# Kernel optimization log

Hardware: AMD Instinct MI355X
Metric: run time of the kernel (lower is better)

Reference implementation:

```python
import jax, jax.numpy as jnp
import numpy as np

B, N, C_IN, C_OUT = 32, 4096, 16, 64
EMB, LINK, WIN = 16, 3, 12


def setup_inputs() -> dict:
    key = jax.random.key(0)
    ks = jax.random.split(key, 7)
    s = lambda k, shape, sc=1.0: jax.random.normal(k, shape, dtype=jnp.float32) * sc
    return {
        "x": s(ks[0], (B, N, C_IN)),
        "x_window": s(ks[1], (B, WIN, N, C_IN)),
        "node_embeddings": s(ks[2], (N, EMB)),
        "weights_pool": s(ks[3], (EMB, LINK, C_IN, C_OUT), 0.1),
        "weights_window": s(ks[4], (EMB, C_IN, C_OUT), 0.1),
        "bias_pool": s(ks[5], (EMB, C_OUT), 0.1),
        "T": s(ks[6], (WIN,), 0.1),
    }


def reference(x, x_window, node_embeddings, weights_pool, weights_window, bias_pool, T):
    # Adaptive adjacency: softmax over rows of relu(E E^T)   [N, N]
    n = node_embeddings.shape[0]
    supports = jax.nn.softmax(
        jax.nn.relu(node_embeddings @ node_embeddings.T), axis=1)
    # Chebyshev polynomial hops: T0=I, T1=A, Tk = 2*A*T(k-1) - T(k-2)
    support_set = [jnp.eye(n, dtype=supports.dtype), supports]
    for _ in range(2, weights_pool.shape[1]):
        support_set.append(2.0 * (supports @ support_set[-1]) - support_set[-2])
    supports_k = jnp.stack(support_set, axis=0)  # [K, N, N]

    # Per-node weight generation from node embeddings
    weights = jnp.einsum('nd,dkio->nkio', node_embeddings, weights_pool)  # [N,K,Cin,Cout]
    bias = node_embeddings @ bias_pool  # [N, Cout]

    # Multi-hop spatial graph convolution
    x_g = jnp.einsum('knm,bmc->bnkc', supports_k, x)  # [B, N, K, Cin]
    x_gconv = jnp.einsum('bnki,nkio->bno', x_g, weights) + bias  # [B, N, Cout]

    # Temporal window transformation: time-mix with T, per-node weights
    x_w = jnp.einsum('btni,t->bni', x_window, T)  # [B, N, Cin]
    w_win = jnp.einsum('nd,dio->nio', node_embeddings, weights_window)  # [N,Cin,Cout]
    x_wconv = jnp.einsum('bni,nio->bno', x_w, w_win)  # [B, N, Cout]

    return x_gconv + x_wconv
```

## Files before the change

kernel.cpp:

```cpp
#include <hip/hip_runtime.h>
#include <hip/hip_bf16.h>

#define NN 4096
#define BB 32
#define CIN 16
#define COUT 64
#define EMB 16
#define KLINK 3
#define WWIN 12
#define BCIN (BB * CIN)
#define KSPLIT 4

typedef unsigned short ushort_t;
typedef __attribute__((ext_vector_type(8))) short bf16x8;
typedef __attribute__((ext_vector_type(4))) float f32x4;
typedef __attribute__((ext_vector_type(4))) unsigned short us4;
typedef __attribute__((ext_vector_type(8))) unsigned short us8;

static __device__ __forceinline__ ushort_t f2bf(float f) {
  union { float f; unsigned u; } v; v.f = f;
  const unsigned r = v.u + 0x7fffu + ((v.u >> 16) & 1u);
  return (ushort_t)(r >> 16);
}
static __device__ __forceinline__ float bf2f(ushort_t u) {
  union { unsigned u; float f; } v; v.u = ((unsigned)u) << 16;
  return v.f;
}

__device__ __forceinline__ void gload16(const void* g, void* l) {
  __builtin_amdgcn_global_load_lds(
      (const __attribute__((address_space(1))) void*)g,
      (__attribute__((address_space(3))) void*)l, 16, 0, 0);
}

__global__ __launch_bounds__(256) void prep_kernel(
    const float* __restrict__ E, const float* __restrict__ Wp,
    const float* __restrict__ Wwp, const float* __restrict__ biasp,
    ushort_t* __restrict__ Ebf, ushort_t* __restrict__ Wpct,
    float* __restrict__ biasn, float* __restrict__ r) {
  const int gid = blockIdx.x * 256 + threadIdx.x;
  if (gid < NN) {
    r[gid] = 0.0f;
    const float* e = E + (size_t)gid * EMB;
    ushort_t* o = Ebf + (size_t)gid * 32;
    #pragma unroll
    for (int d = 0; d < 16; ++d) o[d] = f2bf(e[d]);
    #pragma unroll
    for (int d = 16; d < 32; ++d) o[d] = 0;
  } else if (gid < 2 * NN) {
    const int j = gid - NN;
    const int oo = j >> 6;
    const int i = j & 63;
    const int q = i >> 4;
    const int ii = i & 15;
    ushort_t* w = Wpct + (size_t)j * 32;
    #pragma unroll
    for (int d = 0; d < 16; ++d) {
      float v;
      if (q == 0)
        v = Wp[((size_t)(d * 3 + 0) * 16 + ii) * 64 + oo] -
            Wp[((size_t)(d * 3 + 2) * 16 + ii) * 64 + oo];
      else if (q == 1)
        v = Wp[((size_t)(d * 3 + 1) * 16 + ii) * 64 + oo];
      else if (q == 2)
        v = 2.0f * Wp[((size_t)(d * 3 + 2) * 16 + ii) * 64 + oo];
      else
        v = Wwp[((size_t)d * 16 + ii) * 64 + oo];
      w[d] = f2bf(v);
    }
    #pragma unroll
    for (int d = 16; d < 32; ++d) w[d] = 0;
  } else {
    const int t = gid - 2 * NN;
    if (t < NN * 16) {
      const int n = t >> 4;
      const int o4 = t & 15;
      const float4* bp4 = reinterpret_cast<const float4*>(biasp);
      float4 acc = make_float4(0.f, 0.f, 0.f, 0.f);
      #pragma unroll
      for (int d = 0; d < 16; ++d) {
        const float e = E[(size_t)n * EMB + d];
        const float4 b = bp4[d * 16 + o4];
        acc.x += e * b.x; acc.y += e * b.y; acc.z += e * b.z; acc.w += e * b.w;
      }
      *reinterpret_cast<float4*>(biasn + (size_t)n * 64 + o4 * 4) = acc;
    }
  }
}

__global__ __launch_bounds__(256) void gemm_mfma_kernel(
    const ushort_t* __restrict__ Ag, const ushort_t* __restrict__ Bt,
    ushort_t* __restrict__ Ct, int lda, int ldb, int ldc, int Kdim,
    const float* __restrict__ rowR, const float* __restrict__ colR) {
  __shared__ ushort_t As[128 * 32];
  __shared__ ushort_t Bs[64 * 32];
  const int tid = threadIdx.x;
  const int lane = tid & 63;
  const int wid = tid >> 6;
  const int wr = wid >> 1;
  const int wc = wid & 1;
  const int row0 = blockIdx.y * 128;
  const int col0 = blockIdx.x * 64;

  f32x4 acc[4][2];
  #pragma unroll
  for (int i = 0; i < 4; ++i)
    #pragma unroll
    for (int j = 0; j < 2; ++j) acc[i][j] = (f32x4){0.f, 0.f, 0.f, 0.f};

  const int sr = tid >> 2;
  const int scs = (((tid & 3) ^ (sr & 3)) * 8);
  const ushort_t* agp0 = Ag + (size_t)(row0 + sr) * lda + scs;
  const ushort_t* agp1 = Ag + (size_t)(row0 + 64 + sr) * lda + scs;
  const ushort_t* bgp  = Bt + (size_t)(col0 + sr) * ldb + scs;
  ushort_t* asl0 = &As[tid * 8];
  ushort_t* asl1 = &As[2048 + tid * 8];
  ushort_t* bsl  = &Bs[tid * 8];

  const int kq = (lane >> 4) * 8;
  const int fr = lane & 15;

  for (int kb = 0; kb < Kdim; kb += 32) {
    gload16(agp0 + kb, asl0);
    gload16(agp1 + kb, asl1);
    gload16(bgp + kb, bsl);
    __syncthreads();

    bf16x8 af[4], bfr[2];
    #pragma unroll
    for (int i = 0; i < 4; ++i) {
      const int r = wr * 64 + i * 16 + fr;
      af[i] = *reinterpret_cast<const bf16x8*>(&As[r * 32 + (kq ^ ((r & 3) * 8))]);
    }
    #pragma unroll
    for (int j = 0; j < 2; ++j) {
      const int r = wc * 32 + j * 16 + fr;
      bfr[j] = *reinterpret_cast<const bf16x8*>(&Bs[r * 32 + (kq ^ ((r & 3) * 8))]);
    }
    #pragma unroll
    for (int i = 0; i < 4; ++i)
      #pragma unroll
      for (int j = 0; j < 2; ++j)
        acc[i][j] = __builtin_amdgcn_mfma_f32_16x16x32_bf16(af[i], bfr[j],
                                                            acc[i][j], 0, 0, 0);
    __syncthreads();
  }

  #pragma unroll
  for (int i = 0; i < 4; ++i) {
    const int rg = row0 + wr * 64 + i * 16 + ((lane >> 4) << 2);
    float4 ri = make_float4(1.f, 1.f, 1.f, 1.f);
    if (rowR) {
      const float4 rv = *reinterpret_cast<const float4*>(&rowR[rg]);
      ri.x = 1.0f / rv.x; ri.y = 1.0f / rv.y;
      ri.z = 1.0f / rv.z; ri.w = 1.0f / rv.w;
    }
    #pragma unroll
    for (int j = 0; j < 2; ++j) {
      const int cg = col0 + wc * 32 + j * 16 + (lane & 15);
      float cs = 1.0f;
      if (colR) cs = 1.0f / colR[cg];
      us4 o;
      o.x = f2bf(acc[i][j][0] * ri.x * cs);
      o.y = f2bf(acc[i][j][1] * ri.y * cs);
      o.z = f2bf(acc[i][j][2] * ri.z * cs);
      o.w = f2bf(acc[i][j][3] * ri.w * cs);
      *reinterpret_cast<us4*>(&Ct[(size_t)cg * ldc + rg]) = o;
    }
  }
}

__global__ __launch_bounds__(256) void gemm_splitk_kernel(
    const ushort_t* __restrict__ Ag, const ushort_t* __restrict__ Bt,
    float* __restrict__ Cp, int lda, int ldb, int ldc, int kchunk) {
  __shared__ ushort_t As[128 * 32];
  __shared__ ushort_t Bs[64 * 32];
  const int tid = threadIdx.x;
  const int lane = tid & 63;
  const int wid = tid >> 6;
  const int wr = wid >> 1;
  const int wc = wid & 1;
  const int row0 = blockIdx.y * 128;
  const int col0 = blockIdx.x * 64;
  const int kbase = blockIdx.z * kchunk;

  f32x4 acc[4][2];
  #pragma unroll
  for (int i = 0; i < 4; ++i)
    #pragma unroll
    for (int j = 0; j < 2; ++j) acc[i][j] = (f32x4){0.f, 0.f, 0.f, 0.f};

  const int sr = tid >> 2;
  const int scs = (((tid & 3) ^ (sr & 3)) * 8);
  const ushort_t* agp0 = Ag + (size_t)(row0 + sr) * lda + scs;
  const ushort_t* agp1 = Ag + (size_t)(row0 + 64 + sr) * lda + scs;
  const ushort_t* bgp  = Bt + (size_t)(col0 + sr) * ldb + scs;
  ushort_t* asl0 = &As[tid * 8];
  ushort_t* asl1 = &As[2048 + tid * 8];
  ushort_t* bsl  = &Bs[tid * 8];

  const int kq = (lane >> 4) * 8;
  const int fr = lane & 15;

  for (int kb = kbase; kb < kbase + kchunk; kb += 32) {
    gload16(agp0 + kb, asl0);
    gload16(agp1 + kb, asl1);
    gload16(bgp + kb, bsl);
    __syncthreads();

    bf16x8 af[4], bfr[2];
    #pragma unroll
    for (int i = 0; i < 4; ++i) {
      const int r = wr * 64 + i * 16 + fr;
      af[i] = *reinterpret_cast<const bf16x8*>(&As[r * 32 + (kq ^ ((r & 3) * 8))]);
    }
    #pragma unroll
    for (int j = 0; j < 2; ++j) {
      const int r = wc * 32 + j * 16 + fr;
      bfr[j] = *reinterpret_cast<const bf16x8*>(&Bs[r * 32 + (kq ^ ((r & 3) * 8))]);
    }
    #pragma unroll
    for (int i = 0; i < 4; ++i)
      #pragma unroll
      for (int j = 0; j < 2; ++j)
        acc[i][j] = __builtin_amdgcn_mfma_f32_16x16x32_bf16(af[i], bfr[j],
                                                            acc[i][j], 0, 0, 0);
    __syncthreads();
  }

  float* cpz = Cp + (size_t)blockIdx.z * ((size_t)BCIN * NN);
  #pragma unroll
  for (int i = 0; i < 4; ++i) {
    const int rg = row0 + wr * 64 + i * 16 + ((lane >> 4) << 2);
    #pragma unroll
    for (int j = 0; j < 2; ++j) {
      const int cg = col0 + wc * 32 + j * 16 + (lane & 15);
      *reinterpret_cast<f32x4*>(&cpz[(size_t)cg * ldc + rg]) = acc[i][j];
    }
  }
}

__global__ __launch_bounds__(256) void reduce_splitk_kernel(
    const float* __restrict__ Cp, ushort_t* __restrict__ Ct,
    const float* __restrict__ R, int mode) {
  const size_t e = ((size_t)blockIdx.x * 256 + threadIdx.x) << 2;
  const size_t SS = (size_t)BCIN * NN;
  float4 s = *reinterpret_cast<const float4*>(Cp + e);
  #pragma unroll
  for (int z = 1; z < KSPLIT; ++z) {
    const float4 v = *reinterpret_cast<const float4*>(Cp + (size_t)z * SS + e);
    s.x += v.x; s.y += v.y; s.z += v.z; s.w += v.w;
  }
  if (mode == 0) {
    const float4 rv = *reinterpret_cast<const float4*>(R + (e & (NN - 1)));
    s.x /= rv.x; s.y /= rv.y; s.z /= rv.z; s.w /= rv.w;
  } else {
    const float ri = 1.0f / R[e >> 9];
    s.x *= ri; s.y *= ri; s.z *= ri; s.w *= ri;
  }
  us4 o;
  o.x = f2bf(s.x); o.y = f2bf(s.y); o.z = f2bf(s.z); o.w = f2bf(s.w);
  *reinterpret_cast<us4*>(Ct + e) = o;
}

__global__ __launch_bounds__(256) void pgemm_kernel(
    const ushort_t* __restrict__ Ebf, ushort_t* __restrict__ Pb,
    float* __restrict__ r) {
  __shared__ ushort_t As[128 * 32];
  __shared__ ushort_t Bs[64 * 32];
  const int tid = threadIdx.x;
  const int lane = tid & 63;
  const int wid = tid >> 6;
  const int wr = wid >> 1;
  const int wc = wid & 1;
  const int row0 = blockIdx.y * 128;
  const int col0 = blockIdx.x * 64;

  const int sr = tid >> 2;
  const int scs = (((tid & 3) ^ (sr & 3)) * 8);
  gload16(Ebf + (size_t)(row0 + sr) * 32 + scs, &As[tid * 8]);
  gload16(Ebf + (size_t)(row0 + 64 + sr) * 32 + scs, &As[2048 + tid * 8]);
  gload16(Ebf + (size_t)(col0 + sr) * 32 + scs, &Bs[tid * 8]);
  __syncthreads();

  const int kq = (lane >> 4) * 8;
  const int fr = lane & 15;
  bf16x8 af[4], bfr[2];
  #pragma unroll
  for (int i = 0; i < 4; ++i) {
    const int rr = wr * 64 + i * 16 + fr;
    af[i] = *reinterpret_cast<const bf16x8*>(&As[rr * 32 + (kq ^ ((rr & 3) * 8))]);
  }
  #pragma unroll
  for (int j = 0; j < 2; ++j) {
    const int rr = wc * 32 + j * 16 + fr;
    bfr[j] = *reinterpret_cast<const bf16x8*>(&Bs[rr * 32 + (kq ^ ((rr & 3) * 8))]);
  }
  f32x4 acc[4][2];
  #pragma unroll
  for (int i = 0; i < 4; ++i)
    #pragma unroll
    for (int j = 0; j < 2; ++j) acc[i][j] = (f32x4){0.f, 0.f, 0.f, 0.f};
  #pragma unroll
  for (int i = 0; i < 4; ++i)
    #pragma unroll
    for (int j = 0; j < 2; ++j)
      acc[i][j] = __builtin_amdgcn_mfma_f32_16x16x32_bf16(af[i], bfr[j],
                                                          acc[i][j], 0, 0, 0);

  float pv[4][2][4];
  #pragma unroll
  for (int i = 0; i < 4; ++i) {
    const int rg = row0 + wr * 64 + i * 16 + ((lane >> 4) << 2);
    #pragma unroll
    for (int j = 0; j < 2; ++j) {
      const int cg = col0 + wc * 32 + j * 16 + (lane & 15);
      us4 o;
      #pragma unroll
      for (int q = 0; q < 4; ++q) {
        const float p = __expf(fmaxf(acc[i][j][q], 0.0f) - 16.0f);
        pv[i][j][q] = p;
        o[q] = f2bf(p);
      }
      *reinterpret_cast<us4*>(&Pb[(size_t)cg * NN + rg]) = o;
    }
  }
  #pragma unroll
  for (int i = 0; i < 4; ++i) {
    const int rg = row0 + wr * 64 + i * 16 + ((lane >> 4) << 2);
    #pragma unroll
    for (int q = 0; q < 4; ++q) {
      float s = pv[i][0][q] + pv[i][1][q];
      s += __shfl_xor(s, 1, 64);
      s += __shfl_xor(s, 2, 64);
      s += __shfl_xor(s, 4, 64);
      s += __shfl_xor(s, 8, 64);
      if ((lane & 15) == 0) atomicAdd(&r[rg + q], s);
    }
  }
}

__global__ __launch_bounds__(256) void transpose_x_kernel(
    const float* __restrict__ x, ushort_t* __restrict__ XtT) {
  __shared__ ushort_t T[16][72];
  const int b = blockIdx.y;
  const int m0 = blockIdx.x * 64;
  const int tid = threadIdx.x;
  const int i = tid & 15;
  const int ml = tid >> 4;
  #pragma unroll
  for (int it = 0; it < 4; ++it) {
    const int m = m0 + ml + it * 16;
    T[i][ml + it * 16] = f2bf(x[((size_t)b * NN + m) * CIN + i]);
  }
  __syncthreads();
  if (tid < 128) {
    const int r = tid >> 3;
    const int c8 = (tid & 7) * 8;
    const us8 v = *reinterpret_cast<const us8*>(&T[r][c8]);
    *reinterpret_cast<us8*>(&XtT[(size_t)(b * CIN + r) * NN + m0 + c8]) = v;
  }
}

__global__ __launch_bounds__(256) void transpose_y1_kernel(
    const ushort_t* __restrict__ Y1T, ushort_t* __restrict__ Y1n) {
  __shared__ ushort_t T[64][72];
  const int c0 = blockIdx.x * 64;
  const int r0 = blockIdx.y * 64;
  const int tid = threadIdx.x;
  #pragma unroll
  for (int t = 0; t < 2; ++t) {
    const int lin = tid + t * 256;
    const int row = lin >> 3;
    const int ch = lin & 7;
    const us8 v = *reinterpret_cast<const us8*>(
        Y1T + (size_t)(r0 + row) * NN + c0 + ch * 8);
    *reinterpret_cast<us8*>(&T[row][ch * 8]) = v;
  }
  __syncthreads();
  #pragma unroll
  for (int t = 0; t < 2; ++t) {
    const int lin = tid + t * 256;
    const int cc = lin >> 3;
    const int ch = lin & 7;
    us8 v;
    #pragma unroll
    for (int e = 0; e < 8; ++e) v[e] = T[ch * 8 + e][cc];
    *reinterpret_cast<us8*>(Y1n + (size_t)(c0 + cc) * BCIN + r0 + ch * 8) = v;
  }
}

__global__ __launch_bounds__(256) void time_mix_kernel(
    const float* __restrict__ xw, const float* __restrict__ Tv,
    float* __restrict__ XW) {
  const int idx = blockIdx.x * 256 + threadIdx.x;
  if (idx >= BB * NN * 4) return;
  const int c4 = (idx & 3) << 2;
  const int nn = (idx >> 2) & (NN - 1);
  const int b = idx >> 14;
  float4 acc = make_float4(0.f, 0.f, 0.f, 0.f);
  #pragma unroll
  for (int t = 0; t < WWIN; ++t) {
    const float4 v = *reinterpret_cast<const float4*>(
        xw + (((size_t)b * WWIN + t) * NN + nn) * CIN + c4);
    const float tv = Tv[t];
    acc.x += v.x * tv;
    acc.y += v.y * tv;
    acc.z += v.z * tv;
    acc.w += v.w * tv;
  }
  *reinterpret_cast<float4*>(XW + ((size_t)b * NN + nn) * CIN + c4) = acc;
}

__global__ __launch_bounds__(256) void combine_kernel(
    const float* __restrict__ x, const ushort_t* __restrict__ Y1n,
    const ushort_t* __restrict__ Y2n, const float* __restrict__ XW,
    const ushort_t* __restrict__ Wall, const float* __restrict__ biasn,
    float* __restrict__ out) {
  __shared__ ushort_t lds[4 * 6144];
  const int tid = threadIdx.x;
  const int lane = tid & 63;
  const int w = tid >> 6;
  ushort_t* Wl = lds + w * 6144;
  ushort_t* Vl = Wl + 4096;

  const int perm = ((lane >> 3) << 3) | ((lane & 7) ^ (lane >> 3));
  const int vb = lane >> 1;
  const int i0 = (lane & 1) * 8;

  for (int it = 0; it < 2; ++it) {
    const int n = blockIdx.x * 8 + w * 2 + it;
    asm volatile("s_waitcnt lgkmcnt(0)" ::: "memory");

    const ushort_t* wrow = Wall + (size_t)n * 4096;
    #pragma unroll
    for (int q = 0; q < 8; ++q)
      gload16(wrow + q * 512 + perm * 8, Wl + q * 512);

    const float4* xp = reinterpret_cast<const float4*>(
        x + ((size_t)vb * NN + n) * CIN + i0);
    const float4 xa = xp[0], xb = xp[1];
    const us8 y1 = *reinterpret_cast<const us8*>(Y1n + (size_t)n * BCIN + lane * 8);
    const us8 y2 = *reinterpret_cast<const us8*>(Y2n + (size_t)n * BCIN + lane * 8);
    const float4* xwp = reinterpret_cast<const float4*>(
        XW + ((size_t)vb * NN + n) * CIN + i0);
    const float4 wa = xwp[0], wb = xwp[1];
    us8 xv, wv;
    xv[0] = f2bf(xa.x); xv[1] = f2bf(xa.y); xv[2] = f2bf(xa.z); xv[3] = f2bf(xa.w);
    xv[4] = f2bf(xb.x); xv[5] = f2bf(xb.y); xv[6] = f2bf(xb.z); xv[7] = f2bf(xb.w);
    wv[0] = f2bf(wa.x); wv[1] = f2bf(wa.y); wv[2] = f2bf(wa.z); wv[3] = f2bf(wa.w);
    wv[4] = f2bf(wb.x); wv[5] = f2bf(wb.y); wv[6] = f2bf(wb.z); wv[7] = f2bf(wb.w);
    const int c0 = (lane & 1);
    const int vswz = vb & 7;
    *reinterpret_cast<us8*>(Vl + vb * 64 + (((c0 + 0) ^ vswz) << 3)) = xv;
    *reinterpret_cast<us8*>(Vl + vb * 64 + (((c0 + 2) ^ vswz) << 3)) = y1;
    *reinterpret_cast<us8*>(Vl + vb * 64 + (((c0 + 4) ^ vswz) << 3)) = y2;
    *reinterpret_cast<us8*>(Vl + vb * 64 + (((c0 + 6) ^ vswz) << 3)) = wv;

    f32x4 acc[2][4];
    #pragma unroll
    for (int nt = 0; nt < 4; ++nt) {
      const float bv = biasn[(size_t)n * 64 + nt * 16 + (lane & 15)];
      acc[0][nt] = (f32x4){bv, bv, bv, bv};
      acc[1][nt] = (f32x4){bv, bv, bv, bv};
    }

    asm volatile("s_waitcnt vmcnt(0)" ::: "memory");

    bf16x8 af[2][2], bfr[4][2];
    #pragma unroll
    for (int mt = 0; mt < 2; ++mt)
      #pragma unroll
      for (int kt = 0; kt < 2; ++kt) {
        const int rr = mt * 16 + (lane & 15);
        const int c = kt * 4 + (lane >> 4);
        af[mt][kt] = *reinterpret_cast<const bf16x8*>(
            Vl + rr * 64 + ((c ^ (lane & 7)) << 3));
      }
    #pragma unroll
    for (int nt = 0; nt < 4; ++nt)
      #pragma unroll
      for (int kt = 0; kt < 2; ++kt) {
        const int o = nt * 16 + (lane & 15);
        const int c = kt * 4 + (lane >> 4);
        bfr[nt][kt] = *reinterpret_cast<const bf16x8*>(
            Wl + o * 64 + ((c ^ (lane & 7)) << 3));
      }
    #pragma unroll
    for (int mt = 0; mt < 2; ++mt)
      #pragma unroll
      for (int nt = 0; nt < 4; ++nt)
        #pragma unroll
        for (int kt = 0; kt < 2; ++kt)
          acc[mt][nt] = __builtin_amdgcn_mfma_f32_16x16x32_bf16(
              af[mt][kt], bfr[nt][kt], acc[mt][nt], 0, 0, 0);

    #pragma unroll
    for (int mt = 0; mt < 2; ++mt)
      #pragma unroll
      for (int nt = 0; nt < 4; ++nt) {
        const int o = nt * 16 + (lane & 15);
        #pragma unroll
        for (int rr = 0; rr < 4; ++rr) {
          const int b = mt * 16 + ((lane >> 4) << 2) + rr;
          out[((size_t)b * NN + n) * COUT + o] = acc[mt][nt][rr];
        }
      }
  }
}

extern "C" void kernel_launch(void* const* d_in, const int* in_sizes, int n_in,
                              void* d_out, int out_size, void* d_ws,
                              size_t ws_size, hipStream_t stream) {
  const float* x = (const float*)d_in[0];
  const float* x_window = (const float*)d_in[1];
  const float* E = (const float*)d_in[2];
  const float* Wp = (const float*)d_in[3];
  const float* Wwp = (const float*)d_in[4];
  const float* biasp = (const float*)d_in[5];
  const float* Tv = (const float*)d_in[6];
  float* out = (float*)d_out;

  char* p = (char*)d_ws;
  float* XW = (float*)p;                 p += (size_t)BB * NN * CIN * 4;
  ushort_t* Pb = (ushort_t*)p;           p += (size_t)NN * NN * 2;
  ushort_t* XtT = (ushort_t*)p;          p += (size_t)BCIN * NN * 2;
  ushort_t* Y1T = (ushort_t*)p;          p += (size_t)BCIN * NN * 2;
  ushort_t* Y2n = (ushort_t*)p;          p += (size_t)NN * BCIN * 2;
  ushort_t* Y1n = (ushort_t*)p;          p += (size_t)NN * BCIN * 2;
  ushort_t* Wall = (ushort_t*)p;         p += (size_t)NN * 4096 * 2;
  ushort_t* Ebf = (ushort_t*)p;          p += (size_t)NN * 32 * 2;
  ushort_t* Wpct = (ushort_t*)p;         p += (size_t)NN * 32 * 2;
  float* biasn = (float*)p;              p += (size_t)NN * 64 * 4;
  float* r = (float*)p;                  p += (size_t)NN * 4;
  float* Cpart = (float*)p;              p += (size_t)KSPLIT * BCIN * NN * 4;

  prep_kernel<<<(2 * NN + NN * 16 + 255) / 256, 256, 0, stream>>>(
      E, Wp, Wwp, biasp, Ebf, Wpct, biasn, r);
  gemm_mfma_kernel<<<dim3(NN / 64, NN / 128), 256, 0, stream>>>(
      Wpct, Ebf, Wall, 32, 32, NN, 32, nullptr, nullptr);
  pgemm_kernel<<<dim3(NN / 64, NN / 128), 256, 0, stream>>>(Ebf, Pb, r);
  transpose_x_kernel<<<dim3(NN / 64, BB), 256, 0, stream>>>(x, XtT);
  gemm_splitk_kernel<<<dim3(BCIN / 64, NN / 128, KSPLIT), 256, 0, stream>>>(
      Pb, XtT, Cpart, NN, NN, NN, NN / KSPLIT);
  reduce_splitk_kernel<<<(BCIN * NN / 4) / 256, 256, 0, stream>>>(
      Cpart, Y1T, r, 0);
  gemm_splitk_kernel<<<dim3(NN / 64, BCIN / 128, KSPLIT), 256, 0, stream>>>(
      Y1T, Pb, Cpart, NN, NN, BCIN, NN / KSPLIT);
  reduce_splitk_kernel<<<(BCIN * NN / 4) / 256, 256, 0, stream>>>(
      Cpart, Y2n, r, 1);
  transpose_y1_kernel<<<dim3(NN / 64, BCIN / 64), 256, 0, stream>>>(Y1T, Y1n);
  time_mix_kernel<<<(BB * NN * 4 + 255) / 256, 256, 0, stream>>>(x_window, Tv, XW);
  combine_kernel<<<NN / 8, 256, 0, stream>>>(x, Y1n, Y2n, XW, Wall, biasn, out);
}
```

Baseline: 218.5 us.

## Double-buffer LDS tiles and remap split-K GEMM workgroups across XCDs

The split-K GEMM kernel now keeps two LDS buffers for the A and B tiles. It issues global-to-LDS loads for the next K tile before computing the current one, so memory latency overlaps with MFMA work and one barrier per iteration goes away. It also remaps the linear workgroup id so that blocks dispatched to the same XCD (round-robin by 8) cover contiguous tile ranges, which is meant to improve L2 locality. The cost is doubled LDS use, which can reduce occupancy. The remap assumes the workgroup count is divisible by 8.

```diff
diff --git a/kernel.cpp b/kernel.cpp
--- a/kernel.cpp
+++ b/kernel.cpp
@@ -173,16 +173,25 @@
 __global__ __launch_bounds__(256) void gemm_splitk_kernel(
     const ushort_t* __restrict__ Ag, const ushort_t* __restrict__ Bt,
     float* __restrict__ Cp, int lda, int ldb, int ldc, int kchunk) {
-  __shared__ ushort_t As[128 * 32];
-  __shared__ ushort_t Bs[64 * 32];
+  __shared__ ushort_t As[2][128 * 32];
+  __shared__ ushort_t Bs[2][64 * 32];
   const int tid = threadIdx.x;
   const int lane = tid & 63;
   const int wid = tid >> 6;
   const int wr = wid >> 1;
   const int wc = wid & 1;
-  const int row0 = blockIdx.y * 128;
-  const int col0 = blockIdx.x * 64;
-  const int kbase = blockIdx.z * kchunk;
+
+  const int gx = gridDim.x, gy = gridDim.y;
+  const int nwg = gx * gy * gridDim.z;
+  int L = blockIdx.x + gx * (blockIdx.y + gy * blockIdx.z);
+  L = (L & 7) * (nwg >> 3) + (L >> 3);
+  const int bx = L % gx;
+  const int by = (L / gx) % gy;
+  const int bz = L / (gx * gy);
+
+  const int row0 = by * 128;
+  const int col0 = bx * 64;
+  const int kbase = bz * kchunk;
 
   f32x4 acc[4][2];
   #pragma unroll
@@ -195,29 +204,38 @@
   const ushort_t* agp0 = Ag + (size_t)(row0 + sr) * lda + scs;
   const ushort_t* agp1 = Ag + (size_t)(row0 + 64 + sr) * lda + scs;
   const ushort_t* bgp  = Bt + (size_t)(col0 + sr) * ldb + scs;
-  ushort_t* asl0 = &As[tid * 8];
-  ushort_t* asl1 = &As[2048 + tid * 8];
-  ushort_t* bsl  = &Bs[tid * 8];
 
   const int kq = (lane >> 4) * 8;
   const int fr = lane & 15;
-
-  for (int kb = kbase; kb < kbase + kchunk; kb += 32) {
-    gload16(agp0 + kb, asl0);
-    gload16(agp1 + kb, asl1);
-    gload16(bgp + kb, bsl);
-    __syncthreads();
-
+  const int nt = kchunk >> 5;
+
+  gload16(agp0 + kbase, &As[0][tid * 8]);
+  gload16(agp1 + kbase, &As[0][2048 + tid * 8]);
+  gload16(bgp + kbase, &Bs[0][tid * 8]);
+  __syncthreads();
+
+  int cur = 0;
+  #pragma unroll 2
+  for (int t = 0; t < nt; ++t) {
+    const int nxt = cur ^ 1;
+    if (t + 1 < nt) {
+      const int kb = kbase + (t + 1) * 32;
+      gload16(agp0 + kb, &As[nxt][tid * 8]);
+      gload16(agp1 + kb, &As[nxt][2048 + tid * 8]);
+      gload16(bgp + kb, &Bs[nxt][tid * 8]);
+    }
     bf16x8 af[4], bfr[2];
     #pragma unroll
     for (int i = 0; i < 4; ++i) {
       const int r = wr * 64 + i * 16 + fr;
-      af[i] = *reinterpret_cast<const bf16x8*>(&As[r * 32 + (kq ^ ((r & 3) * 8))]);
+      af[i] = *reinterpret_cast<const bf16x8*>(
+          &As[cur][r * 32 + (kq ^ ((r & 3) * 8))]);
     }
     #pragma unroll
     for (int j = 0; j < 2; ++j) {
       const int r = wc * 32 + j * 16 + fr;
-      bfr[j] = *reinterpret_cast<const bf16x8*>(&Bs[r * 32 + (kq ^ ((r & 3) * 8))]);
+      bfr[j] = *reinterpret_cast<const bf16x8*>(
+          &Bs[cur][r * 32 + (kq ^ ((r & 3) * 8))]);
     }
     #pragma unroll
     for (int i = 0; i < 4; ++i)
@@ -226,9 +244,10 @@
         acc[i][j] = __builtin_amdgcn_mfma_f32_16x16x32_bf16(af[i], bfr[j],
                                                             acc[i][j], 0, 0, 0);
     __syncthreads();
-  }
-
-  float* cpz = Cp + (size_t)blockIdx.z * ((size_t)BCIN * NN);
+    cur = nxt;
+  }
+
+  float* cpz = Cp + (size_t)bz * ((size_t)BCIN * NN);
   #pragma unroll
   for (int i = 0; i < 4; ++i) {
     const int rg = row0 + wr * 64 + i * 16 + ((lane >> 4) << 2);
```

Measured after the change: 194.5 us. 1.12x faster.
